# Optimization experiments

Measured on AMD Instinct MI355X. Metric: run time of the kernel, lower is better.

## Reference

```python
import jax, jax.numpy as jnp
import numpy as np

N, E, B = 200000, 6400000, 128
IN_LOCAL, IN_GLOBAL, HIDDEN, NUM_CLASSES = 16, 8, 32, 2


def setup_inputs() -> dict:
    key = jax.random.key(0)
    ks = jax.random.split(key, 16)
    inp = {
        "x_local": jax.random.normal(ks[0], (N, IN_LOCAL), dtype=jnp.float32),
        "x_global": jax.random.normal(ks[1], (B, IN_GLOBAL), dtype=jnp.float32),
        "batch": jnp.sort(jax.random.randint(ks[2], (N,), 0, B, dtype=jnp.int64)),
        "edge_index": jax.random.randint(ks[3], (2, E), 0, N, dtype=jnp.int64),
        # encoder params
        "W_local": jax.random.normal(ks[4], (IN_LOCAL, HIDDEN), jnp.float32) / np.sqrt(IN_LOCAL),
        "b_local": jnp.zeros((HIDDEN,), jnp.float32),
        "W_global": jax.random.normal(ks[5], (IN_GLOBAL, HIDDEN), jnp.float32) / np.sqrt(IN_GLOBAL),
        "b_global": jnp.zeros((HIDDEN,), jnp.float32),
        "W_mix": jax.random.normal(ks[6], (3 * HIDDEN, HIDDEN), jnp.float32) / np.sqrt(3 * HIDDEN),
        "b_mix": jnp.zeros((HIDDEN,), jnp.float32),
        # GNN layer params
        "W_msg": jax.random.normal(ks[7], (HIDDEN, HIDDEN), jnp.float32) / np.sqrt(HIDDEN),
        "b_msg": jnp.zeros((HIDDEN,), jnp.float32),
        "W_self": jax.random.normal(ks[8], (HIDDEN, HIDDEN), jnp.float32) / np.sqrt(HIDDEN),
        "b_self": jnp.zeros((HIDDEN,), jnp.float32),
        # output head
        "W_out": jax.random.normal(ks[9], (HIDDEN, NUM_CLASSES), jnp.float32) / np.sqrt(HIDDEN),
        "b_out": jnp.zeros((NUM_CLASSES,), jnp.float32),
    }
    return inp


def reference(x_local, x_global, batch, edge_index,
              W_local, b_local, W_global, b_global, W_mix, b_mix,
              W_msg, b_msg, W_self, b_self, W_out, b_out):
    n = x_local.shape[0]
    # --- MixedSelectivityNodeEncoder ---
    h_local = jax.nn.relu(x_local @ W_local + b_local)            # [N,H]
    h_global_graph = jax.nn.relu(x_global @ W_global + b_global)  # [B,H]
    h_global = h_global_graph[batch]                              # gather -> [N,H]
    h_int = h_local * h_global
    h_cat = jnp.concatenate([h_local, h_global, h_int], axis=-1)  # [N,3H]
    h0 = jax.nn.relu(h_cat @ W_mix + b_mix)                       # [N,H]
    # --- GNN layer with self loops, add aggregation ---
    loops = jnp.arange(n, dtype=edge_index.dtype)
    src = jnp.concatenate([edge_index[0], loops])                 # [E+N]
    dst = jnp.concatenate([edge_index[1], loops])                 # [E+N]
    msg = jax.nn.relu(h0[src] @ W_msg + b_msg)                    # [E+N,H]
    aggr = jax.ops.segment_sum(msg, dst, num_segments=n)          # [N,H]
    h = jax.nn.relu(aggr + h0 @ W_self + b_self)                  # [N,H]
    # --- output head ---
    return h @ W_out + b_out                                      # [N,C]
```

## Files before the change

kernel.cpp:

```cpp
#include <hip/hip_runtime.h>

#define N_NODES  200000
#define N_EDGES  6400000
#define NGRAPH   128
#define H        32
#define ZROW     N_NODES

#define BNODES   256
#define NBUCK    782
#define P_BLOCKS 256
#define EPB      25000
#define SORT_CAP 10240
#define BSPLIT   391

typedef unsigned short ushort_t;

__device__ __forceinline__ ushort_t f32_to_bf16_rne(float f) {
    unsigned u = __float_as_uint(f);
    unsigned r = (u + 0x7fffu + ((u >> 16) & 1u)) >> 16;
    return (ushort_t)r;
}

__global__ __launch_bounds__(256) void k_node_enc(
        const float* __restrict__ xl,
        const int*   __restrict__ batch,
        const float* __restrict__ xg,   const float* __restrict__ Wg,
        const float* __restrict__ bg,
        const float* __restrict__ Wl,   const float* __restrict__ bl,
        const float* __restrict__ Wmix, const float* __restrict__ bmix,
        const float* __restrict__ Wmsg, const float* __restrict__ bmsg,
        const float* __restrict__ Wself,const float* __restrict__ bself,
        ushort_t* __restrict__ mb, float* __restrict__ s) {
    int n0 = blockIdx.x * 256 + threadIdx.x;
    bool valid = (n0 < N_NODES);
    int n = valid ? n0 : (N_NODES - 1);

    float xv[16];
    {
        const float4* p = (const float4*)(xl + (size_t)n * 16);
        float4 a = p[0], b = p[1], c = p[2], d = p[3];
        xv[0]=a.x; xv[1]=a.y; xv[2]=a.z; xv[3]=a.w;
        xv[4]=b.x; xv[5]=b.y; xv[6]=b.z; xv[7]=b.w;
        xv[8]=c.x; xv[9]=c.y; xv[10]=c.z; xv[11]=c.w;
        xv[12]=d.x; xv[13]=d.y; xv[14]=d.z; xv[15]=d.w;
    }
    float gvv[8];
    {
        int gb = batch[n];
        const float4* q = (const float4*)(xg + (size_t)gb * 8);
        float4 a = q[0], b = q[1];
        gvv[0]=a.x; gvv[1]=a.y; gvv[2]=a.z; gvv[3]=a.w;
        gvv[4]=b.x; gvv[5]=b.y; gvv[6]=b.z; gvv[7]=b.w;
    }

    float hl[32], hg[32], hi[32];
#pragma unroll
    for (int t4 = 0; t4 < 8; ++t4) {
        float4 al = ((const float4*)bl)[t4];
        float4 ag = ((const float4*)bg)[t4];
#pragma unroll
        for (int k = 0; k < 16; ++k) {
            float4 w = ((const float4*)(Wl + k * H))[t4];
            al.x = fmaf(xv[k], w.x, al.x); al.y = fmaf(xv[k], w.y, al.y);
            al.z = fmaf(xv[k], w.z, al.z); al.w = fmaf(xv[k], w.w, al.w);
        }
#pragma unroll
        for (int k = 0; k < 8; ++k) {
            float4 w = ((const float4*)(Wg + k * H))[t4];
            ag.x = fmaf(gvv[k], w.x, ag.x); ag.y = fmaf(gvv[k], w.y, ag.y);
            ag.z = fmaf(gvv[k], w.z, ag.z); ag.w = fmaf(gvv[k], w.w, ag.w);
        }
        hl[t4*4+0] = fmaxf(al.x, 0.f); hl[t4*4+1] = fmaxf(al.y, 0.f);
        hl[t4*4+2] = fmaxf(al.z, 0.f); hl[t4*4+3] = fmaxf(al.w, 0.f);
        hg[t4*4+0] = fmaxf(ag.x, 0.f); hg[t4*4+1] = fmaxf(ag.y, 0.f);
        hg[t4*4+2] = fmaxf(ag.z, 0.f); hg[t4*4+3] = fmaxf(ag.w, 0.f);
    }
#pragma unroll
    for (int k = 0; k < 32; ++k) hi[k] = hl[k] * hg[k];

    float h0[32];
#pragma unroll
    for (int t4 = 0; t4 < 8; ++t4) {
        float4 acc = ((const float4*)bmix)[t4];
#pragma unroll
        for (int k = 0; k < 32; ++k) {
            float4 w = ((const float4*)(Wmix + k * H))[t4];
            acc.x = fmaf(hl[k], w.x, acc.x); acc.y = fmaf(hl[k], w.y, acc.y);
            acc.z = fmaf(hl[k], w.z, acc.z); acc.w = fmaf(hl[k], w.w, acc.w);
        }
#pragma unroll
        for (int k = 0; k < 32; ++k) {
            float4 w = ((const float4*)(Wmix + (32 + k) * H))[t4];
            acc.x = fmaf(hg[k], w.x, acc.x); acc.y = fmaf(hg[k], w.y, acc.y);
            acc.z = fmaf(hg[k], w.z, acc.z); acc.w = fmaf(hg[k], w.w, acc.w);
        }
#pragma unroll
        for (int k = 0; k < 32; ++k) {
            float4 w = ((const float4*)(Wmix + (64 + k) * H))[t4];
            acc.x = fmaf(hi[k], w.x, acc.x); acc.y = fmaf(hi[k], w.y, acc.y);
            acc.z = fmaf(hi[k], w.z, acc.z); acc.w = fmaf(hi[k], w.w, acc.w);
        }
        h0[t4*4+0] = fmaxf(acc.x, 0.f); h0[t4*4+1] = fmaxf(acc.y, 0.f);
        h0[t4*4+2] = fmaxf(acc.z, 0.f); h0[t4*4+3] = fmaxf(acc.w, 0.f);
    }

#pragma unroll
    for (int t4 = 0; t4 < 8; ++t4) {
        float4 am = ((const float4*)bmsg)[t4];
        float4 as = ((const float4*)bself)[t4];
#pragma unroll
        for (int k = 0; k < 32; ++k) {
            float4 wm = ((const float4*)(Wmsg + k * H))[t4];
            float4 ws = ((const float4*)(Wself + k * H))[t4];
            am.x = fmaf(h0[k], wm.x, am.x); am.y = fmaf(h0[k], wm.y, am.y);
            am.z = fmaf(h0[k], wm.z, am.z); am.w = fmaf(h0[k], wm.w, am.w);
            as.x = fmaf(h0[k], ws.x, as.x); as.y = fmaf(h0[k], ws.y, as.y);
            as.z = fmaf(h0[k], ws.z, as.z); as.w = fmaf(h0[k], ws.w, as.w);
        }
        if (valid) {
            unsigned d0 = (unsigned)f32_to_bf16_rne(fmaxf(am.x, 0.f))
                        | ((unsigned)f32_to_bf16_rne(fmaxf(am.y, 0.f)) << 16);
            unsigned d1 = (unsigned)f32_to_bf16_rne(fmaxf(am.z, 0.f))
                        | ((unsigned)f32_to_bf16_rne(fmaxf(am.w, 0.f)) << 16);
            ((unsigned*)(mb + (size_t)n * H))[t4*2+0] = d0;
            ((unsigned*)(mb + (size_t)n * H))[t4*2+1] = d1;
            ((float4*)(s + (size_t)n * H))[t4] = as;
        }
    }

    if (n0 == N_NODES) {
        float4 z = make_float4(0.f, 0.f, 0.f, 0.f);
        float4* p = (float4*)(mb + (size_t)ZROW * H);
        p[0] = z; p[1] = z; p[2] = z; p[3] = z;
    }
}

__global__ __launch_bounds__(1024) void k_pcount(const int* __restrict__ ei,
                                                 int* __restrict__ gcnt) {
    __shared__ int cnt[NBUCK];
    int t = threadIdx.x, blk = blockIdx.x;
    for (int i = t; i < NBUCK; i += 1024) cnt[i] = 0;
    __syncthreads();
    int e1 = (blk + 1) * EPB;
    for (int e = blk * EPB + t; e < e1; e += 1024)
        atomicAdd(&cnt[ei[N_EDGES + e] >> 8], 1);
    __syncthreads();
    for (int i = t; i < NBUCK; i += 1024)
        gcnt[i * P_BLOCKS + blk] = cnt[i];
}

__global__ void k_blocksum_g(const int* __restrict__ gcnt, int* __restrict__ bsum) {
    int b = blockIdx.x, t = threadIdx.x;
    int v = gcnt[b * P_BLOCKS + t];
#pragma unroll
    for (int off = 32; off >= 1; off >>= 1)
        v += __shfl_down(v, off, 64);
    __shared__ int w4[4];
    if ((t & 63) == 0) w4[t >> 6] = v;
    __syncthreads();
    if (t == 0) bsum[b] = w4[0] + w4[1] + w4[2] + w4[3];
}

__global__ void k_scan_bsums_g(const int* __restrict__ bsum, int* __restrict__ boff) {
    __shared__ int sd[1024];
    int t = threadIdx.x;
    sd[t] = (t < NBUCK) ? bsum[t] : 0;
    __syncthreads();
#pragma unroll
    for (int off = 1; off < 1024; off <<= 1) {
        int v = (t >= off) ? sd[t - off] : 0;
        __syncthreads();
        sd[t] += v;
        __syncthreads();
    }
    if (t < NBUCK) boff[t] = (t == 0) ? 0 : sd[t - 1];
}

__global__ void k_make_cursor_g(int* __restrict__ gcnt, const int* __restrict__ boff) {
    __shared__ int sd[P_BLOCKS];
    int b = blockIdx.x, t = threadIdx.x, i = b * P_BLOCKS + t;
    int c = gcnt[i];
    sd[t] = c;
    __syncthreads();
#pragma unroll
    for (int off = 1; off < P_BLOCKS; off <<= 1) {
        int v = (t >= off) ? sd[t - off] : 0;
        __syncthreads();
        sd[t] += v;
        __syncthreads();
    }
    gcnt[i] = boff[b] + sd[t] - c;
}

__global__ __launch_bounds__(1024) void k_pscatter(const int* __restrict__ ei,
                                                   const int* __restrict__ goff,
                                                   unsigned int* __restrict__ ebuf) {
    __shared__ int cur[NBUCK];
    int t = threadIdx.x, blk = blockIdx.x;
    for (int i = t; i < NBUCK; i += 1024) cur[i] = goff[i * P_BLOCKS + blk];
    __syncthreads();
    int e0 = blk * EPB, e1 = e0 + EPB;
#pragma unroll 1
    for (int half = 0; half < 2; ++half) {
        for (int e = e0 + t; e < e1; e += 1024) {
            int dst = __builtin_nontemporal_load(ei + N_EDGES + e);
            int b   = dst >> 8;
            if ((b < BSPLIT) != (half == 0)) continue;
            unsigned src = (unsigned)__builtin_nontemporal_load(ei + e);
            int pos = atomicAdd(&cur[b], 1);
            ebuf[pos] = (src << 8) | (unsigned)(dst & 255);
        }
    }
}

__global__ __launch_bounds__(512) void k_bsort(const int* __restrict__ goff,
                                               unsigned int* __restrict__ ebuf,
                                               int* __restrict__ row_start) {
    __shared__ unsigned sorted[SORT_CAP];
    __shared__ int cnt[BNODES];
    __shared__ int off[BNODES];
    __shared__ int cur[BNODES];
    int tid = threadIdx.x, b = blockIdx.x;

    int bs = goff[b * P_BLOCKS];
    int be = (b == NBUCK - 1) ? N_EDGES : goff[(b + 1) * P_BLOCKS];

    if (tid < BNODES) cnt[tid] = 0;
    __syncthreads();

    for (int j = bs + tid; j < be; j += 512)
        atomicAdd(&cnt[ebuf[j] & 255], 1);
    __syncthreads();

    if (tid < BNODES) off[tid] = cnt[tid];
    __syncthreads();
#pragma unroll
    for (int d = 1; d < BNODES; d <<= 1) {
        int v = (tid < BNODES && tid >= d) ? off[tid - d] : 0;
        __syncthreads();
        if (tid < BNODES) off[tid] += v;
        __syncthreads();
    }
    if (tid < BNODES) cur[tid] = off[tid] - cnt[tid];
    __syncthreads();

    for (int j = bs + tid; j < be; j += 512) {
        unsigned pk = ebuf[j];
        int pos = atomicAdd(&cur[pk & 255], 1);
        sorted[pos] = pk;
    }
    __syncthreads();

    int sz = be - bs;
    for (int i = tid; i < sz; i += 512)
        ebuf[bs + i] = sorted[i] >> 8;

    if (tid < BNODES) {
        int n = b * BNODES + tid;
        if (n <= N_NODES)
            row_start[n] = bs + (off[tid] - cnt[tid]);
    }
}

__global__ __launch_bounds__(256) void k_aggr_final(
        const int* __restrict__ row_start,
        const int* __restrict__ csr,
        const ushort_t* __restrict__ mb, const float* __restrict__ s,
        const float* __restrict__ Wout, const float* __restrict__ bout,
        float* __restrict__ out) {
    int tid = threadIdx.x;
    int grp = tid >> 4;
    int t2  = tid & 15;
    int n   = blockIdx.x * 16 + grp;

    int start = row_start[n];
    int end   = row_start[n + 1];

    const unsigned* mb32 = (const unsigned*)mb;

    float alo[8], ahi[8];
#pragma unroll
    for (int k = 0; k < 8; ++k) { alo[k] = 0.f; ahi[k] = 0.f; }

    for (int j = start; j < end; j += 8) {
        int idx[8];
#pragma unroll
        for (int k = 0; k < 8; ++k) {
            int src = csr[j + k];
            idx[k] = (j + k < end) ? src : ZROW;
        }
        unsigned d[8];
#pragma unroll
        for (int k = 0; k < 8; ++k)
            d[k] = mb32[idx[k] * 16 + t2];
#pragma unroll
        for (int k = 0; k < 8; ++k) {
            alo[k] += __uint_as_float(d[k] << 16);
            ahi[k] += __uint_as_float(d[k] & 0xffff0000u);
        }
    }
    float accl = ((alo[0]+alo[1])+(alo[2]+alo[3]))+((alo[4]+alo[5])+(alo[6]+alo[7]));
    float acch = ((ahi[0]+ahi[1])+(ahi[2]+ahi[3]))+((ahi[4]+ahi[5])+(ahi[6]+ahi[7]));

    unsigned dself = mb32[(size_t)n * 16 + t2];
    float2 sv = ((const float2*)(s + (size_t)n * H))[t2];
    float hlo = fmaxf(accl + __uint_as_float(dself << 16) + sv.x, 0.f);
    float hhi = fmaxf(acch + __uint_as_float(dself & 0xffff0000u) + sv.y, 0.f);

    float4 w = ((const float4*)Wout)[t2];
    float p0 = fmaf(hlo, w.x, hhi * w.z);
    float p1 = fmaf(hlo, w.y, hhi * w.w);
#pragma unroll
    for (int off = 8; off >= 1; off >>= 1) {
        p0 += __shfl_down(p0, off, 16);
        p1 += __shfl_down(p1, off, 16);
    }
    if (t2 == 0) {
        out[n * 2 + 0] = p0 + bout[0];
        out[n * 2 + 1] = p1 + bout[1];
    }
}

extern "C" void kernel_launch(void* const* d_in, const int* in_sizes, int n_in,
                              void* d_out, int out_size, void* d_ws, size_t ws_size,
                              hipStream_t stream) {
    const float* xl    = (const float*)d_in[0];
    const float* xg    = (const float*)d_in[1];
    const int*   batch = (const int*)  d_in[2];
    const int*   ei    = (const int*)  d_in[3];
    const float* Wl    = (const float*)d_in[4];
    const float* bl    = (const float*)d_in[5];
    const float* Wg    = (const float*)d_in[6];
    const float* bg    = (const float*)d_in[7];
    const float* Wmix  = (const float*)d_in[8];
    const float* bmix  = (const float*)d_in[9];
    const float* Wmsg  = (const float*)d_in[10];
    const float* bmsg  = (const float*)d_in[11];
    const float* Wself = (const float*)d_in[12];
    const float* bself = (const float*)d_in[13];
    const float* Wout  = (const float*)d_in[14];
    const float* bout  = (const float*)d_in[15];
    float* out = (float*)d_out;

    float*    s    = (float*)d_ws;
    ushort_t* mb   = (ushort_t*)(s + (size_t)N_NODES * H);
    int*      gcnt = (int*)(mb + (size_t)(N_NODES + 1) * H);
    int*      bsum = gcnt + (size_t)NBUCK * P_BLOCKS;
    int*      boff = bsum + NBUCK;
    int*      row_start = boff + NBUCK;
    unsigned int* ebuf = (unsigned int*)(row_start + N_NODES + 2);

    k_node_enc<<<(N_NODES + 256) / 256, 256, 0, stream>>>(xl, batch, xg, Wg, bg,
                                                          Wl, bl, Wmix, bmix,
                                                          Wmsg, bmsg, Wself, bself,
                                                          mb, s);

    k_pcount<<<P_BLOCKS, 1024, 0, stream>>>(ei, gcnt);
    k_blocksum_g<<<NBUCK, P_BLOCKS, 0, stream>>>(gcnt, bsum);
    k_scan_bsums_g<<<1, 1024, 0, stream>>>(bsum, boff);
    k_make_cursor_g<<<NBUCK, P_BLOCKS, 0, stream>>>(gcnt, boff);
    k_pscatter<<<P_BLOCKS, 1024, 0, stream>>>(ei, gcnt, ebuf);

    k_bsort<<<NBUCK, 512, 0, stream>>>(gcnt, ebuf, row_start);

    k_aggr_final<<<N_NODES / 16, 256, 0, stream>>>(row_start, (const int*)ebuf,
                                                   mb, s, Wout, bout, out);
}
```

Measured before the change: 389.9 us.

## Fuse bucket sort with aggregation and merge edge counting into encoder launch

The per-bucket sort kernel now goes on to do the neighbour aggregation and output head itself. It reads source indices straight from the LDS-sorted buffer, so the sorted CSR is never written back to global memory and row_start disappears. The edge-destination histogram runs as extra blocks of the node-encoder launch, which lets both independent stages share one grid and drops a launch. In exchange, aggregation parallelism falls from many small blocks to one 512-thread block per 256-node bucket, and the 40KB LDS footprint limits occupancy for a latency-bound gather. The unrolled reads of the sorted LDS array can also run up to seven entries past a node's edge range.

```diff
diff --git a/kernel.cpp b/kernel.cpp
--- a/kernel.cpp
+++ b/kernel.cpp
@@ -12,6 +12,7 @@
 #define EPB      25000
 #define SORT_CAP 10240
 #define BSPLIT   391
+#define ENC_BLOCKS 783
 
 typedef unsigned short ushort_t;
 
@@ -21,7 +22,7 @@
     return (ushort_t)r;
 }
 
-__global__ __launch_bounds__(256) void k_node_enc(
+__global__ __launch_bounds__(256) void k_phase1(
         const float* __restrict__ xl,
         const int*   __restrict__ batch,
         const float* __restrict__ xg,   const float* __restrict__ Wg,
@@ -30,7 +31,25 @@
         const float* __restrict__ Wmix, const float* __restrict__ bmix,
         const float* __restrict__ Wmsg, const float* __restrict__ bmsg,
         const float* __restrict__ Wself,const float* __restrict__ bself,
-        ushort_t* __restrict__ mb, float* __restrict__ s) {
+        const int* __restrict__ ei,
+        ushort_t* __restrict__ mb, float* __restrict__ s,
+        int* __restrict__ gcnt) {
+    __shared__ int cnt[NBUCK];
+
+    if (blockIdx.x >= ENC_BLOCKS) {
+        int blk = blockIdx.x - ENC_BLOCKS;
+        int t = threadIdx.x;
+        for (int i = t; i < NBUCK; i += 256) cnt[i] = 0;
+        __syncthreads();
+        int e1 = (blk + 1) * EPB;
+        for (int e = blk * EPB + t; e < e1; e += 256)
+            atomicAdd(&cnt[__builtin_nontemporal_load(ei + N_EDGES + e) >> 8], 1);
+        __syncthreads();
+        for (int i = t; i < NBUCK; i += 256)
+            gcnt[i * P_BLOCKS + blk] = cnt[i];
+        return;
+    }
+
     int n0 = blockIdx.x * 256 + threadIdx.x;
     bool valid = (n0 < N_NODES);
     int n = valid ? n0 : (N_NODES - 1);
@@ -133,20 +152,6 @@
         float4* p = (float4*)(mb + (size_t)ZROW * H);
         p[0] = z; p[1] = z; p[2] = z; p[3] = z;
     }
-}
-
-__global__ __launch_bounds__(1024) void k_pcount(const int* __restrict__ ei,
-                                                 int* __restrict__ gcnt) {
-    __shared__ int cnt[NBUCK];
-    int t = threadIdx.x, blk = blockIdx.x;
-    for (int i = t; i < NBUCK; i += 1024) cnt[i] = 0;
-    __syncthreads();
-    int e1 = (blk + 1) * EPB;
-    for (int e = blk * EPB + t; e < e1; e += 1024)
-        atomicAdd(&cnt[ei[N_EDGES + e] >> 8], 1);
-    __syncthreads();
-    for (int i = t; i < NBUCK; i += 1024)
-        gcnt[i * P_BLOCKS + blk] = cnt[i];
 }
 
 __global__ void k_blocksum_g(const int* __restrict__ gcnt, int* __restrict__ bsum) {
@@ -213,9 +218,12 @@
     }
 }
 
-__global__ __launch_bounds__(512) void k_bsort(const int* __restrict__ goff,
-                                               unsigned int* __restrict__ ebuf,
-                                               int* __restrict__ row_start) {
+__global__ __launch_bounds__(512) void k_bsort_aggr(
+        const int* __restrict__ goff,
+        const unsigned int* __restrict__ ebuf,
+        const ushort_t* __restrict__ mb, const float* __restrict__ s,
+        const float* __restrict__ Wout, const float* __restrict__ bout,
+        float* __restrict__ out) {
     __shared__ unsigned sorted[SORT_CAP];
     __shared__ int cnt[BNODES];
     __shared__ int off[BNODES];
@@ -251,73 +259,58 @@
     }
     __syncthreads();
 
-    int sz = be - bs;
-    for (int i = tid; i < sz; i += 512)
-        ebuf[bs + i] = sorted[i] >> 8;
-
-    if (tid < BNODES) {
-        int n = b * BNODES + tid;
-        if (n <= N_NODES)
-            row_start[n] = bs + (off[tid] - cnt[tid]);
-    }
-}
-
-__global__ __launch_bounds__(256) void k_aggr_final(
-        const int* __restrict__ row_start,
-        const int* __restrict__ csr,
-        const ushort_t* __restrict__ mb, const float* __restrict__ s,
-        const float* __restrict__ Wout, const float* __restrict__ bout,
-        float* __restrict__ out) {
-    int tid = threadIdx.x;
+    const unsigned* mb32 = (const unsigned*)mb;
     int grp = tid >> 4;
     int t2  = tid & 15;
-    int n   = blockIdx.x * 16 + grp;
-
-    int start = row_start[n];
-    int end   = row_start[n + 1];
-
-    const unsigned* mb32 = (const unsigned*)mb;
-
-    float alo[8], ahi[8];
-#pragma unroll
-    for (int k = 0; k < 8; ++k) { alo[k] = 0.f; ahi[k] = 0.f; }
-
-    for (int j = start; j < end; j += 8) {
-        int idx[8];
-#pragma unroll
-        for (int k = 0; k < 8; ++k) {
-            int src = csr[j + k];
-            idx[k] = (j + k < end) ? src : ZROW;
-        }
-        unsigned d[8];
-#pragma unroll
-        for (int k = 0; k < 8; ++k)
-            d[k] = mb32[idx[k] * 16 + t2];
-#pragma unroll
-        for (int k = 0; k < 8; ++k) {
-            alo[k] += __uint_as_float(d[k] << 16);
-            ahi[k] += __uint_as_float(d[k] & 0xffff0000u);
-        }
-    }
-    float accl = ((alo[0]+alo[1])+(alo[2]+alo[3]))+((alo[4]+alo[5])+(alo[6]+alo[7]));
-    float acch = ((ahi[0]+ahi[1])+(ahi[2]+ahi[3]))+((ahi[4]+ahi[5])+(ahi[6]+ahi[7]));
-
-    unsigned dself = mb32[(size_t)n * 16 + t2];
-    float2 sv = ((const float2*)(s + (size_t)n * H))[t2];
-    float hlo = fmaxf(accl + __uint_as_float(dself << 16) + sv.x, 0.f);
-    float hhi = fmaxf(acch + __uint_as_float(dself & 0xffff0000u) + sv.y, 0.f);
-
     float4 w = ((const float4*)Wout)[t2];
-    float p0 = fmaf(hlo, w.x, hhi * w.z);
-    float p1 = fmaf(hlo, w.y, hhi * w.w);
-#pragma unroll
-    for (int off = 8; off >= 1; off >>= 1) {
-        p0 += __shfl_down(p0, off, 16);
-        p1 += __shfl_down(p1, off, 16);
-    }
-    if (t2 == 0) {
-        out[n * 2 + 0] = p0 + bout[0];
-        out[n * 2 + 1] = p1 + bout[1];
+    float b0 = bout[0], b1 = bout[1];
+
+    for (int nn = grp; nn < BNODES; nn += 32) {
+        int n = b * BNODES + nn;
+        if (n >= N_NODES) break;
+        int jend   = off[nn];
+        int jstart = jend - cnt[nn];
+
+        float alo[8], ahi[8];
+#pragma unroll
+        for (int k = 0; k < 8; ++k) { alo[k] = 0.f; ahi[k] = 0.f; }
+
+        for (int j = jstart; j < jend; j += 8) {
+            int idx[8];
+#pragma unroll
+            for (int k = 0; k < 8; ++k) {
+                unsigned pk = sorted[j + k];
+                idx[k] = (j + k < jend) ? (int)(pk >> 8) : ZROW;
+            }
+            unsigned d[8];
+#pragma unroll
+            for (int k = 0; k < 8; ++k)
+                d[k] = mb32[idx[k] * 16 + t2];
+#pragma unroll
+            for (int k = 0; k < 8; ++k) {
+                alo[k] += __uint_as_float(d[k] << 16);
+                ahi[k] += __uint_as_float(d[k] & 0xffff0000u);
+            }
+        }
+        float accl = ((alo[0]+alo[1])+(alo[2]+alo[3]))+((alo[4]+alo[5])+(alo[6]+alo[7]));
+        float acch = ((ahi[0]+ahi[1])+(ahi[2]+ahi[3]))+((ahi[4]+ahi[5])+(ahi[6]+ahi[7]));
+
+        unsigned dself = mb32[(size_t)n * 16 + t2];
+        float2 sv = ((const float2*)(s + (size_t)n * H))[t2];
+        float hlo = fmaxf(accl + __uint_as_float(dself << 16) + sv.x, 0.f);
+        float hhi = fmaxf(acch + __uint_as_float(dself & 0xffff0000u) + sv.y, 0.f);
+
+        float p0 = fmaf(hlo, w.x, hhi * w.z);
+        float p1 = fmaf(hlo, w.y, hhi * w.w);
+#pragma unroll
+        for (int o = 8; o >= 1; o >>= 1) {
+            p0 += __shfl_down(p0, o, 16);
+            p1 += __shfl_down(p1, o, 16);
+        }
+        if (t2 == 0) {
+            out[n * 2 + 0] = p0 + b0;
+            out[n * 2 + 1] = p1 + b1;
+        }
     }
 }
 
@@ -347,22 +340,16 @@
     int*      gcnt = (int*)(mb + (size_t)(N_NODES + 1) * H);
     int*      bsum = gcnt + (size_t)NBUCK * P_BLOCKS;
     int*      boff = bsum + NBUCK;
-    int*      row_start = boff + NBUCK;
-    unsigned int* ebuf = (unsigned int*)(row_start + N_NODES + 2);
-
-    k_node_enc<<<(N_NODES + 256) / 256, 256, 0, stream>>>(xl, batch, xg, Wg, bg,
-                                                          Wl, bl, Wmix, bmix,
-                                                          Wmsg, bmsg, Wself, bself,
-                                                          mb, s);
-
-    k_pcount<<<P_BLOCKS, 1024, 0, stream>>>(ei, gcnt);
+    unsigned int* ebuf = (unsigned int*)(boff + NBUCK);
+
+    k_phase1<<<ENC_BLOCKS + P_BLOCKS, 256, 0, stream>>>(
+        xl, batch, xg, Wg, bg, Wl, bl, Wmix, bmix,
+        Wmsg, bmsg, Wself, bself, ei, mb, s, gcnt);
+
     k_blocksum_g<<<NBUCK, P_BLOCKS, 0, stream>>>(gcnt, bsum);
     k_scan_bsums_g<<<1, 1024, 0, stream>>>(bsum, boff);
     k_make_cursor_g<<<NBUCK, P_BLOCKS, 0, stream>>>(gcnt, boff);
     k_pscatter<<<P_BLOCKS, 1024, 0, stream>>>(ei, gcnt, ebuf);
 
-    k_bsort<<<NBUCK, 512, 0, stream>>>(gcnt, ebuf, row_start);
-
-    k_aggr_final<<<N_NODES / 16, 256, 0, stream>>>(row_start, (const int*)ebuf,
-                                                   mb, s, Wout, bout, out);
-}
+    k_bsort_aggr<<<NBUCK, 512, 0, stream>>>(gcnt, ebuf, mb, s, Wout, bout, out);
+}
```

New measurement: 422.5 us. 8.4% more time.
